# Optimization experiments

Measured on AMD Instinct MI355X. Metric: run time of the kernel, lower is better.

The kernel has to match this reference:

```python
import jax, jax.numpy as jnp
import numpy as np

D_MODEL = 1024
D_STATE = 32
DT_MIN, DT_MAX = 1e-3, 1e-1
L_LEN = 2048


def setup_inputs() -> dict:
    key = jax.random.key(0)
    k1, k2, k3 = jax.random.split(key, 3)
    # log_dt ~ U[log(dt_min), log(dt_max)]
    log_dt = jax.random.uniform(k1, (D_MODEL,), dtype=jnp.float32) \
        * (np.log(DT_MAX) - np.log(DT_MIN)) + np.log(DT_MIN)
    # log_A_real = log(0.5), A_imag = pi * arange(N) per channel
    log_A_real = jnp.full((D_MODEL, D_STATE), np.log(0.5), dtype=jnp.float32)
    A_imag = jnp.broadcast_to(np.pi * jnp.arange(D_STATE, dtype=jnp.float32),
                              (D_MODEL, D_STATE)).copy()
    # B = 1 + 0j ; C ~ complex normal (real/imag each N(0,1))
    B_re = jnp.ones((D_MODEL, D_STATE), dtype=jnp.float32)
    B_im = jnp.zeros((D_MODEL, D_STATE), dtype=jnp.float32)
    C_re = jax.random.normal(k2, (D_MODEL, D_STATE), dtype=jnp.float32)
    C_im = jax.random.normal(k3, (D_MODEL, D_STATE), dtype=jnp.float32)
    return {"log_dt": log_dt, "log_A_real": log_A_real, "A_imag": A_imag,
            "B_re": B_re, "B_im": B_im, "C_re": C_re, "C_im": C_im,
            "L": L_LEN}


def reference(log_dt, log_A_real, A_imag, B_re, B_im, C_re, C_im, L):
    # ZOH discretization of diagonal SSM, then Vandermonde kernel.
    dt = jnp.exp(log_dt)                                  # (H,)
    A = -jnp.exp(log_A_real) + 1j * A_imag                # (H, N) complex
    dtA = A * dt[:, None]                                 # (H, N)
    A_bar = jnp.exp(dtA)                                  # (H, N)
    B = B_re + 1j * B_im
    C = C_re + 1j * C_im
    B_bar = (A_bar - 1.0) / A * B                         # (H, N)
    t = jnp.arange(L)                                     # (L,)
    # A_bar^t = exp(t * dtA) for integer t (avoids complex pow branch issues,
    # mathematically identical to torch.pow(A_bar, t) here)
    A_bar_pow = jnp.exp(dtA[:, :, None] * t[None, None, :])  # (H, N, L)
    K = jnp.einsum('hn,hnl->hl', C * B_bar, A_bar_pow)       # weighted reduce
    return K.real
```

## Files before the change

kernel.cpp:

```cpp
#include <hip/hip_runtime.h>
#include <hip/hip_bf16.h>

#define H_MODEL 1024
#define N_STATE 32
#define L_LEN   2048
#define BLK     512
#define QL      128
#define GSTEP   16
#define NPQ     (N_STATE / 4)
#define NPAIR   (GSTEP / 2)

typedef float v2f __attribute__((ext_vector_type(2)));

__global__ __launch_bounds__(BLK, 8) void s4d_kernel(
    const float* __restrict__ log_dt,
    const float* __restrict__ log_A_real,
    const float* __restrict__ A_imag,
    const float* __restrict__ B_re,
    const float* __restrict__ B_im,
    const float* __restrict__ C_re,
    const float* __restrict__ C_im,
    float* __restrict__ out)
{
    const int h = blockIdx.x;

    __shared__ float4 s_c1[N_STATE];
    __shared__ float4 s_c2[N_STATE];
    __shared__ float  s_part[3][QL][GSTEP + 1];

    if (threadIdx.x < N_STATE) {
        const int n   = threadIdx.x;
        const int idx = h * N_STATE + n;
        const float dt   = __expf(log_dt[h]);
        const float a_re = -__expf(log_A_real[idx]);
        const float a_im = A_imag[idx];
        const float dre  = a_re * dt;
        const float dim  = a_im * dt;

        const float er = __expf(dre);
        float sn, cs;
        __sincosf(dim, &sn, &cs);
        const float abar_re = er * cs;
        const float abar_im = er * sn;

        const float num_re = abar_re - 1.0f;
        const float num_im = abar_im;
        const float inv_d  = 1.0f / (a_re * a_re + a_im * a_im);
        const float q_re   = (num_re * a_re + num_im * a_im) * inv_d;
        const float q_im   = (num_im * a_re - num_re * a_im) * inv_d;

        const float br = B_re[idx], bi = B_im[idx];
        const float bb_re = q_re * br - q_im * bi;
        const float bb_im = q_re * bi + q_im * br;
        const float cr = C_re[idx], ci = C_im[idx];
        const float wre = cr * bb_re - ci * bb_im;
        const float wim = cr * bb_im + ci * bb_re;

        const float erB = __expf(dre * (float)QL);
        float snB, csB;
        __sincosf(dim * (float)QL, &snB, &csB);
        const float Er = erB * csB;
        const float Ei = erB * snB;
        s_c1[n] = make_float4(dre, dim, wre, wim);
        s_c2[n] = make_float4(Er, Ei, 2.0f * Er, -(Er * Er + Ei * Ei));
    }
    __syncthreads();

    const int   q  = threadIdx.x >> 7;
    const int   l  = threadIdx.x & (QL - 1);
    const int   nb = q * NPQ;
    const float t  = (float)l;

    v2f acc[NPAIR];
    #pragma unroll
    for (int j = 0; j < NPAIR; ++j) acc[j] = (v2f){0.0f, 0.0f};

    #pragma unroll 2
    for (int jn = 0; jn < NPQ; ++jn) {
        const float4 c1 = s_c1[nb + jn];
        const float4 c2 = s_c2[nb + jn];

        const float a2 = __builtin_fmaf(c2.z, c2.z, c2.w + c2.w);
        const float b2 = -(c2.w * c2.w);
        const v2f A2 = {a2, a2};
        const v2f B2 = {b2, b2};

        const float er = __expf(c1.x * t);
        float sn, cs;
        __sincosf(c1.y * t, &sn, &cs);
        const float z0r = er * (c1.z * cs - c1.w * sn);
        const float z0i = er * (c1.w * cs + c1.z * sn);

        const float r0 = z0r;
        const float r1 = z0r * c2.x - z0i * c2.y;
        const float r2 = __builtin_fmaf(c2.z, r1, c2.w * r0);
        const float r3 = __builtin_fmaf(c2.z, r2, c2.w * r1);

        v2f P0 = {r0, r1};
        v2f P1 = {r2, r3};
        acc[0] += P0;
        acc[1] += P1;
        #pragma unroll
        for (int k = 2; k < NPAIR; ++k) {
            const v2f Pn = __builtin_elementwise_fma(A2, P1, B2 * P0);
            acc[k] += Pn;
            P0 = P1; P1 = Pn;
        }
    }

    if (q != 0) {
        #pragma unroll
        for (int j = 0; j < NPAIR; ++j) {
            s_part[q - 1][l][2 * j]     = acc[j].x;
            s_part[q - 1][l][2 * j + 1] = acc[j].y;
        }
    }
    __syncthreads();
    if (q == 0) {
        #pragma unroll
        for (int b = 0; b < 3; ++b) {
            #pragma unroll
            for (int j = 0; j < NPAIR; ++j) {
                acc[j].x += s_part[b][l][2 * j];
                acc[j].y += s_part[b][l][2 * j + 1];
            }
        }
        float* orow = out + h * L_LEN + l;
        #pragma unroll
        for (int j = 0; j < NPAIR; ++j) {
            orow[(2 * j) * QL]     = acc[j].x;
            orow[(2 * j + 1) * QL] = acc[j].y;
        }
    }
}

extern "C" void kernel_launch(void* const* d_in, const int* in_sizes, int n_in,
                              void* d_out, int out_size, void* d_ws, size_t ws_size,
                              hipStream_t stream) {
    const float* log_dt     = (const float*)d_in[0];
    const float* log_A_real = (const float*)d_in[1];
    const float* A_imag     = (const float*)d_in[2];
    const float* B_re       = (const float*)d_in[3];
    const float* B_im       = (const float*)d_in[4];
    const float* C_re       = (const float*)d_in[5];
    const float* C_im       = (const float*)d_in[6];
    float* out              = (float*)d_out;

    s4d_kernel<<<dim3(H_MODEL), dim3(BLK), 0, stream>>>(
        log_dt, log_A_real, A_imag, B_re, B_im, C_re, C_im, out);
}
```

Measured before the change: 13.50 us.

## Use raw hardware exp2/sin/cos and spread final reduction across all warps

Prescales the per-state decay and phase constants by log2(e) and 1/(2π) so the inner loop can call v_exp_f32 and v_sin/v_cos_f32 directly on a fract-reduced argument, skipping the range reduction inside __expf/__sincosf. The cross-quarter reduction now has every quarter write its partials to shared memory, after which each quarter sums four partials for a quarter of the output columns. Before, one quarter did all the summing and stores. This balances the epilogue but adds shared-memory traffic, and accuracy depends on fract precision at large t·phase.

```diff
diff --git a/kernel.cpp b/kernel.cpp
--- a/kernel.cpp
+++ b/kernel.cpp
@@ -11,6 +11,13 @@
 #define NPAIR   (GSTEP / 2)
 
 typedef float v2f __attribute__((ext_vector_type(2)));
+
+__device__ __forceinline__ float vsin_rev(float x) {
+    float r; asm("v_sin_f32 %0, %1" : "=v"(r) : "v"(x)); return r;
+}
+__device__ __forceinline__ float vcos_rev(float x) {
+    float r; asm("v_cos_f32 %0, %1" : "=v"(r) : "v"(x)); return r;
+}
 
 __global__ __launch_bounds__(BLK, 8) void s4d_kernel(
     const float* __restrict__ log_dt,
@@ -26,7 +33,7 @@
 
     __shared__ float4 s_c1[N_STATE];
     __shared__ float4 s_c2[N_STATE];
-    __shared__ float  s_part[3][QL][GSTEP + 1];
+    __shared__ float  s_part[4][QL][GSTEP + 1];
 
     if (threadIdx.x < N_STATE) {
         const int n   = threadIdx.x;
@@ -61,7 +68,8 @@
         __sincosf(dim * (float)QL, &snB, &csB);
         const float Er = erB * csB;
         const float Ei = erB * snB;
-        s_c1[n] = make_float4(dre, dim, wre, wim);
+        s_c1[n] = make_float4(dre * 1.44269504088896341f,
+                              dim * 0.15915494309189535f, wre, wim);
         s_c2[n] = make_float4(Er, Ei, 2.0f * Er, -(Er * Er + Ei * Ei));
     }
     __syncthreads();
@@ -85,14 +93,15 @@
         const v2f A2 = {a2, a2};
         const v2f B2 = {b2, b2};
 
-        const float er = __expf(c1.x * t);
-        float sn, cs;
-        __sincosf(c1.y * t, &sn, &cs);
-        const float z0r = er * (c1.z * cs - c1.w * sn);
-        const float z0i = er * (c1.w * cs + c1.z * sn);
+        const float er = __builtin_amdgcn_exp2f(c1.x * t);
+        const float uf = __builtin_amdgcn_fractf(c1.y * t);
+        const float sn = vsin_rev(uf);
+        const float cs = vcos_rev(uf);
+        const float z0r = er * __builtin_fmaf(c1.z, cs, -(c1.w * sn));
+        const float z0i = er * __builtin_fmaf(c1.w, cs,  (c1.z * sn));
 
         const float r0 = z0r;
-        const float r1 = z0r * c2.x - z0i * c2.y;
+        const float r1 = __builtin_fmaf(z0r, c2.x, -(z0i * c2.y));
         const float r2 = __builtin_fmaf(c2.z, r1, c2.w * r0);
         const float r3 = __builtin_fmaf(c2.z, r2, c2.w * r1);
 
@@ -108,28 +117,22 @@
         }
     }
 
-    if (q != 0) {
-        #pragma unroll
-        for (int j = 0; j < NPAIR; ++j) {
-            s_part[q - 1][l][2 * j]     = acc[j].x;
-            s_part[q - 1][l][2 * j + 1] = acc[j].y;
-        }
+    #pragma unroll
+    for (int j = 0; j < NPAIR; ++j) {
+        s_part[q][l][2 * j]     = acc[j].x;
+        s_part[q][l][2 * j + 1] = acc[j].y;
     }
     __syncthreads();
-    if (q == 0) {
-        #pragma unroll
-        for (int b = 0; b < 3; ++b) {
-            #pragma unroll
-            for (int j = 0; j < NPAIR; ++j) {
-                acc[j].x += s_part[b][l][2 * j];
-                acc[j].y += s_part[b][l][2 * j + 1];
-            }
-        }
+
+    {
+        const int k0 = q * (GSTEP / 4);
         float* orow = out + h * L_LEN + l;
         #pragma unroll
-        for (int j = 0; j < NPAIR; ++j) {
-            orow[(2 * j) * QL]     = acc[j].x;
-            orow[(2 * j + 1) * QL] = acc[j].y;
+        for (int j = 0; j < GSTEP / 4; ++j) {
+            const int k = k0 + j;
+            const float s = (s_part[0][l][k] + s_part[1][l][k])
+                          + (s_part[2][l][k] + s_part[3][l][k]);
+            orow[k * QL] = s;
         }
     }
 }
```

Result: faster. 13.08 us (median of 2 runs) (-3.1%).
